# Optimization experiments

Measured on AMD Instinct MI355X. Metric: run time of the kernel, lower is better.

The kernel has to match this reference:

```python
import math
import jax, jax.numpy as jnp
import numpy as np

EMBED_DIM = 1024
NUM_HEADS = 16
FACTOR = 5


def setup_inputs() -> dict:
    key = jax.random.key(0)
    kx, kw, kb, kow, kob = jax.random.split(key, 5)
    B, S, E = 8, 4096, EMBED_DIM
    scale = 1.0 / math.sqrt(E)
    x = jax.random.normal(kx, (B, S, E), dtype=jnp.float32)
    # nn.MultiheadAttention params: packed in_proj (q,k,v) and out_proj
    in_proj_w = jax.random.uniform(kw, (3 * E, E), dtype=jnp.float32, minval=-scale, maxval=scale)
    in_proj_b = jnp.zeros((3 * E,), dtype=jnp.float32)
    out_w = jax.random.uniform(kow, (E, E), dtype=jnp.float32, minval=-scale, maxval=scale)
    out_b = jnp.zeros((E,), dtype=jnp.float32)
    return {"x": x, "in_proj_w": in_proj_w, "in_proj_b": in_proj_b, "out_w": out_w, "out_b": out_b}


def reference(x, in_proj_w, in_proj_b, out_w, out_b):
    B, S, E = x.shape
    H = NUM_HEADS
    hd = E // H
    k = max(1, int(FACTOR * math.log(S + 1)))
    k = min(k, S)

    # top-k queries by L2 norm of each token
    energy = jnp.linalg.norm(x, axis=-1)            # [B, S]
    _, topk_idx = jax.lax.top_k(energy, k)          # [B, k]

    q_tok = jnp.take_along_axis(x, topk_idx[..., None], axis=1)  # [B, k, E]

    Wq, Wk, Wv = jnp.split(in_proj_w, 3, axis=0)    # each [E, E]
    bq, bk, bv = jnp.split(in_proj_b, 3, axis=0)

    q = (q_tok @ Wq.T + bq).reshape(B, k, H, hd)    # [B, k, H, hd]
    kk = (x @ Wk.T + bk).reshape(B, S, H, hd)       # [B, S, H, hd]
    v = (x @ Wv.T + bv).reshape(B, S, H, hd)

    scores = jnp.einsum("bqhd,bshd->bhqs", q, kk) / math.sqrt(hd)
    attn = jax.nn.softmax(scores, axis=-1)          # [B, H, k, S]
    ctx = jnp.einsum("bhqs,bshd->bqhd", attn, v).reshape(B, k, E)
    out_sel = ctx @ out_w.T + out_b                 # [B, k, E]

    # default value for non-selected positions: per-batch mean of x
    default = jnp.mean(x, axis=1)                   # [B, E]
    result = jnp.broadcast_to(default[:, None, :], (B, S, E))
    batch_ar = jnp.arange(B)[:, None]
    result = result.at[batch_ar, topk_idx].set(out_sel)
    return result
```

## Files before the change

### kernel.cpp

```cpp
#include <hip/hip_runtime.h>

using u16 = unsigned short;
using u32 = unsigned int;
using u64 = unsigned long long;
typedef __attribute__((ext_vector_type(8))) short s16x8;
typedef __attribute__((ext_vector_type(4))) short s16x4;
typedef __attribute__((ext_vector_type(4))) float f32x4;

__device__ __forceinline__ float bf2f(u16 u){ return __uint_as_float(((u32)u)<<16); }
__device__ __forceinline__ u16 f2bf(float f){
  u32 u = __float_as_uint(f);
  u += 0x7fffu + ((u>>16)&1u);
  return (u16)(u>>16);
}
__device__ __forceinline__ void gl_lds16(const void* g, void* l){
  __builtin_amdgcn_global_load_lds((const __attribute__((address_space(1))) void*)g,
                                   (__attribute__((address_space(3))) void*)l, 16, 0, 0);
}

__global__ __launch_bounds__(256) void k_cvt_all(const float* __restrict__ ipw, const float* __restrict__ ipb,
                                                 const float* __restrict__ outw, const float* __restrict__ outb,
                                                 u16* __restrict__ ipwb, u16* __restrict__ ipbb,
                                                 u16* __restrict__ outwb, u16* __restrict__ outbb){
  int bid = blockIdx.x;
  const float* src; u16* dst; int n; int base;
  if (bid < 3072){ src=ipw; dst=ipwb; n=3145728; base=bid; }
  else if (bid < 3075){ src=ipb; dst=ipbb; n=3072; base=bid-3072; }
  else if (bid < 4099){ src=outw; dst=outwb; n=1048576; base=bid-3075; }
  else { src=outb; dst=outbb; n=1024; base=0; }
  int i = (base*256 + threadIdx.x)*4;
  if (i >= n) return;
  float4 v = *(const float4*)(src + i);
  s16x4 o;
  o[0]=(short)f2bf(v.x); o[1]=(short)f2bf(v.y); o[2]=(short)f2bf(v.z); o[3]=(short)f2bf(v.w);
  *(s16x4*)(dst + i) = o;
}

__global__ __launch_bounds__(256) void k_prep_x(const float* __restrict__ x, u16* __restrict__ xb, float* __restrict__ energy){
  int tok = blockIdx.x*4 + (threadIdx.x>>6);
  int lane = threadIdx.x & 63;
  const float* p = x + (size_t)tok*1024 + lane*16;
  float4 a[4];
  #pragma unroll
  for (int j=0;j<4;++j) a[j] = ((const float4*)p)[j];
  float s = 0.f;
  s16x8 o0, o1;
  #pragma unroll
  for (int j=0;j<2;++j){
    o0[j*4+0]=(short)f2bf(a[j].x); o0[j*4+1]=(short)f2bf(a[j].y);
    o0[j*4+2]=(short)f2bf(a[j].z); o0[j*4+3]=(short)f2bf(a[j].w);
  }
  #pragma unroll
  for (int j=0;j<2;++j){
    o1[j*4+0]=(short)f2bf(a[2+j].x); o1[j*4+1]=(short)f2bf(a[2+j].y);
    o1[j*4+2]=(short)f2bf(a[2+j].z); o1[j*4+3]=(short)f2bf(a[2+j].w);
  }
  #pragma unroll
  for (int j=0;j<4;++j){
    s += a[j].x*a[j].x + a[j].y*a[j].y + a[j].z*a[j].z + a[j].w*a[j].w;
  }
  u16* xo = xb + (size_t)tok*1024 + lane*16;
  *(s16x8*)xo = o0;
  *(s16x8*)(xo+8) = o1;
  #pragma unroll
  for (int off=32; off; off>>=1) s += __shfl_xor(s, off);
  if (lane==0) energy[tok] = s;
}

__global__ __launch_bounds__(256) void k_colsum(const u16* __restrict__ xb, float* __restrict__ colsum){
  int b = blockIdx.x, sc = blockIdx.y;
  int t = threadIdx.x;
  float acc[4] = {0.f,0.f,0.f,0.f};
  for (int s = sc*128; s < sc*128+128; ++s){
    s16x4 v = *(const s16x4*)(xb + ((size_t)b*4096 + s)*1024 + t*4);
    #pragma unroll
    for (int i=0;i<4;++i) acc[i] += bf2f((u16)v[i]);
  }
  #pragma unroll
  for (int i=0;i<4;++i) atomicAdd(&colsum[b*1024 + t*4 + i], acc[i]);
}

__global__ __launch_bounds__(256) void k_topk(const float* __restrict__ energy, int* __restrict__ topk, int* __restrict__ sel){
  int b = blockIdx.x, t = threadIdx.x;
  int lane = t & 63, wid = t >> 6;
  __shared__ u64 wmax[4];
  __shared__ u64 winner;
  u64 v[16];
  #pragma unroll
  for (int i=0;i<16;++i){
    u32 tok = i*256 + t;
    float e = energy[b*4096 + tok];
    v[i] = ((u64)__float_as_uint(e) << 32) | (u32)(~tok);
    sel[b*4096 + tok] = -1;
  }
  __syncthreads();
  for (int it=0; it<41; ++it){
    u64 m = v[0];
    #pragma unroll
    for (int i=1;i<16;++i) m = v[i] > m ? v[i] : m;
    #pragma unroll
    for (int off=32; off; off>>=1){
      u64 o = __shfl_xor(m, off);
      m = o > m ? o : m;
    }
    if (lane==0) wmax[wid] = m;
    __syncthreads();
    if (t==0){
      u64 g = wmax[0];
      #pragma unroll
      for (int w=1;w<4;++w) g = wmax[w] > g ? wmax[w] : g;
      winner = g;
      u32 tok = (~(u32)g) & 4095u;
      topk[b*64+it] = (int)tok;
      sel[b*4096 + tok] = it;
    }
    __syncthreads();
    u32 wtok = (~(u32)winner) & 4095u;
    #pragma unroll
    for (int i=0;i<16;++i){
      if ((u32)(i*256 + t) == wtok) v[i] = 0;
    }
  }
}

__global__ __launch_bounds__(256) void k_gather_q(const float* __restrict__ x, const int* __restrict__ topk,
                                                  u16* __restrict__ Aq){
  int b = blockIdx.x, qi = blockIdx.y, t = threadIdx.x;
  size_t dst = ((size_t)(b*48+qi))*1024 + t*4;
  if (qi >= 41){ s16x4 z = {0,0,0,0}; *(s16x4*)&Aq[dst] = z; return; }
  int tok = topk[b*64+qi];
  float4 v = *(const float4*)(x + ((size_t)b*4096 + tok)*1024 + t*4);
  s16x4 o;
  o[0]=(short)f2bf(v.x); o[1]=(short)f2bf(v.y); o[2]=(short)f2bf(v.z); o[3]=(short)f2bf(v.w);
  *(s16x4*)&Aq[dst] = o;
}

__global__ __launch_bounds__(256) void k_gemm(const u16* __restrict__ A, const u16* __restrict__ Bk,
                                              const u16* __restrict__ Bv,
                                              const u16* __restrict__ biask, const u16* __restrict__ biasv,
                                              u16* __restrict__ C, int nbn, int ncols, int half, float cscale){
  __shared__ u16 As[128*64];
  __shared__ u16 Bs[128*64];
  const int tid = threadIdx.x;
  const int bn = blockIdx.x % nbn;
  const int bm = blockIdx.x / nbn;
  const int m0 = bm*128, n0 = bn*128;
  const u16* Bbase  = (n0 < half) ? (Bk + (size_t)n0*1024) : (Bv + (size_t)(n0-half)*1024);
  const u16* biasp  = (n0 < half) ? (biask + n0) : (biasv + (n0-half));
  const int lane = tid & 63;
  const int wave = tid >> 6;
  const int wr = wave >> 1, wc = wave & 1;
  const int fr = lane & 15;
  const int fq = lane >> 4;
  f32x4 acc[4][4] = {};
  for (int k0 = 0; k0 < 1024; k0 += 64){
    __syncthreads();
    #pragma unroll
    for (int j=0;j<4;++j){
      int idx = j*256 + tid;
      int r = idx>>3; int cc = (idx&7)*8;
      gl_lds16(A + (size_t)(m0+r)*1024 + k0 + cc, &As[r*64+cc]);
    }
    #pragma unroll
    for (int j=0;j<4;++j){
      int idx = j*256 + tid;
      int r = idx>>3; int cc = (idx&7)*8;
      gl_lds16(Bbase + (size_t)r*1024 + k0 + cc, &Bs[r*64+cc]);
    }
    __syncthreads();
    #pragma unroll
    for (int kk=0; kk<64; kk+=32){
      s16x8 af[4], bfv[4];
      #pragma unroll
      for (int m=0;m<4;++m) af[m] = *(const s16x8*)&As[(wr*64 + m*16 + fr)*64 + kk + fq*8];
      #pragma unroll
      for (int n=0;n<4;++n) bfv[n] = *(const s16x8*)&Bs[(wc*64 + n*16 + fr)*64 + kk + fq*8];
      #pragma unroll
      for (int m=0;m<4;++m)
        #pragma unroll
        for (int n=0;n<4;++n)
          acc[m][n] = __builtin_amdgcn_mfma_f32_16x16x32_bf16(af[m], bfv[n], acc[m][n], 0,0,0);
    }
  }
  #pragma unroll
  for (int n=0;n<4;++n){
    int cl = wc*64 + n*16 + fr;
    int col = n0 + cl;
    float bvv = bf2f(biasp[cl]);
    #pragma unroll
    for (int m=0;m<4;++m){
      int rowb = m0 + wr*64 + m*16 + fq*4;
      f32x4 v = acc[m][n];
      #pragma unroll
      for (int i=0;i<4;++i)
        C[(size_t)(rowb+i)*ncols + col] = f2bf((v[i]+bvv)*cscale);
    }
  }
}

__device__ __forceinline__ void stageA2(const u16* __restrict__ A, int m0, int k0, u16* ldsSlot, int tid){
  #pragma unroll
  for (int j=0;j<4;++j){
    int idx = j*512 + tid;
    int row = idx>>3;
    int chunk = (tid&7) ^ (row&7);
    gl_lds16(A + (size_t)(m0+row)*1024 + k0 + chunk*8, ldsSlot + (size_t)idx*8);
  }
}
__device__ __forceinline__ void stageB2(const u16* __restrict__ B, int k0, u16* ldsSlot, int tid){
  #pragma unroll
  for (int j=0;j<2;++j){
    int idx = j*512 + tid;
    int row = idx>>3;
    int chunk = (tid&7) ^ (row&7);
    gl_lds16(B + (size_t)row*1024 + k0 + chunk*8, ldsSlot + 16384 + (size_t)idx*8);
  }
}
__device__ __forceinline__ s16x8 fragA2(const u16* slot, int row, int k2, int fq){
  int chunk = (fq + k2*4) ^ (row&7);
  return *(const s16x8*)(slot + row*64 + chunk*8);
}
__device__ __forceinline__ s16x8 fragB2(const u16* slot, int row, int k2, int fq){
  int chunk = (fq + k2*4) ^ (row&7);
  return *(const s16x8*)(slot + 16384 + row*64 + chunk*8);
}

__global__ __launch_bounds__(512) void k_kvgemm2(const u16* __restrict__ A, const u16* __restrict__ Bk,
                                                 const u16* __restrict__ Bv,
                                                 const u16* __restrict__ biask, const u16* __restrict__ biasv,
                                                 u16* __restrict__ C){
  __shared__ u16 lds[3*24576];
  const int tid = threadIdx.x;
  const int sbid = (blockIdx.x & 7)*256 + (blockIdx.x >> 3);
  const int bn = sbid & 15;
  const int bm = sbid >> 4;
  const int m0 = bm*256, n0 = bn*128;
  const u16* Bbase = (bn < 8) ? (Bk + (size_t)n0*1024) : (Bv + (size_t)(n0-1024)*1024);
  const u16* biasp = (bn < 8) ? (biask + n0) : (biasv + (n0-1024));
  const int lane = tid & 63, wid = tid >> 6;
  const int wm = wid >> 1, wn = wid & 1;
  const int fr = lane & 15, fq = lane >> 4;
  f32x4 acc[4][4] = {};

  stageA2(A, m0, 0, lds, tid);        stageB2(Bbase, 0, lds, tid);
  stageA2(A, m0, 64, lds+24576, tid); stageB2(Bbase, 64, lds+24576, tid);
  asm volatile("s_waitcnt vmcnt(6)" ::: "memory");
  __builtin_amdgcn_s_barrier();

  for (int t=0; t<16; ++t){
    const u16* slot = lds + (t%3)*24576;
    u16* nslot = (u16*)lds + ((t+2)%3)*24576;
    if (t < 14){ stageA2(A, m0, (t+2)*64, nslot, tid); stageB2(Bbase, (t+2)*64, nslot, tid); }
    s16x8 afr[4][2], bfr[4][2];
    #pragma unroll
    for (int m=0;m<4;++m)
      #pragma unroll
      for (int k2=0;k2<2;++k2)
        afr[m][k2] = fragA2(slot, wm*64 + m*16 + fr, k2, fq);
    #pragma unroll
    for (int n=0;n<4;++n)
      #pragma unroll
      for (int k2=0;k2<2;++k2)
        bfr[n][k2] = fragB2(slot, wn*64 + n*16 + fr, k2, fq);
    __builtin_amdgcn_s_setprio(1);
    #pragma unroll
    for (int m=0;m<4;++m)
      #pragma unroll
      for (int n=0;n<4;++n)
        #pragma unroll
        for (int k2=0;k2<2;++k2)
          acc[m][n] = __builtin_amdgcn_mfma_f32_16x16x32_bf16(afr[m][k2], bfr[n][k2], acc[m][n], 0,0,0);
    __builtin_amdgcn_s_setprio(0);
    if (t < 14){
      asm volatile("s_waitcnt vmcnt(6)" ::: "memory");
    } else if (t == 14){
      asm volatile("s_waitcnt vmcnt(0)" ::: "memory");
    }
    __builtin_amdgcn_s_barrier();
  }

  #pragma unroll
  for (int n=0;n<4;++n){
    int cl = wn*64 + n*16 + fr;
    int col = n0 + cl;
    float bvv = bf2f(biasp[cl]);
    #pragma unroll
    for (int m=0;m<4;++m){
      int rowb = m0 + wm*64 + m*16 + fq*4;
      f32x4 v = acc[m][n];
      #pragma unroll
      for (int i=0;i<4;++i)
        C[(size_t)(rowb+i)*2048 + col] = f2bf(v[i]+bvv);
    }
  }
}

__global__ __launch_bounds__(64) void k_attn(const u16* __restrict__ qb, const u16* __restrict__ KV,
                                             float* __restrict__ part_ctx, float* __restrict__ part_ml,
                                             int G, int hg0, int ncols, int half, int nt, int NSP){
  const int b = blockIdx.x / G, hl = blockIdx.x % G;
  const int h = hg0 + hl;
  const int bh = b*16 + h;
  const int sp = blockIdx.y;
  const int lane = threadIdx.x;
  const int fr = lane & 15, fq = lane >> 4;
  __shared__ u16 k_lds[64*72];
  __shared__ u16 v_lds[64*72];
  __shared__ u16 p_lds[48*72];
  s16x8 af[3][2];
  #pragma unroll
  for (int m=0;m<3;++m)
    #pragma unroll
    for (int kk=0;kk<2;++kk)
      af[m][kk] = *(const s16x8*)(qb + ((size_t)(b*48 + m*16 + fr))*1024 + h*64 + kk*32 + fq*8);
  f32x4 acc_o[3][4] = {};
  float m_run[3][4], l_run[3][4];
  #pragma unroll
  for (int m=0;m<3;++m)
    #pragma unroll
    for (int i=0;i<4;++i){ m_run[m][i] = -3e38f; l_run[m][i] = 0.f; }

  for (int it=0; it<nt; ++it){
    int s0 = (sp*nt + it)*64;
    __syncthreads();
    #pragma unroll
    for (int j=0;j<8;++j){
      int r = j*8 + (lane>>3);
      int sg = (lane&7)*8;
      const u16* kp = KV + ((size_t)(b*4096 + s0 + r))*ncols + hl*64 + sg;
      *(s16x8*)&k_lds[r*72+sg] = *(const s16x8*)kp;
      *(s16x8*)&v_lds[r*72+sg] = *(const s16x8*)(kp+half);
    }
    __syncthreads();
    f32x4 sc4[3][4] = {};
    #pragma unroll
    for (int kk=0;kk<2;++kk){
      s16x8 bk[4];
      #pragma unroll
      for (int n=0;n<4;++n)
        bk[n] = *(const s16x8*)&k_lds[(n*16+fr)*72 + kk*32 + fq*8];
      #pragma unroll
      for (int m=0;m<3;++m)
        #pragma unroll
        for (int n=0;n<4;++n)
          sc4[m][n] = __builtin_amdgcn_mfma_f32_16x16x32_bf16(af[m][kk], bk[n], sc4[m][n], 0,0,0);
    }
    #pragma unroll
    for (int m=0;m<3;++m){
      #pragma unroll
      for (int i=0;i<4;++i){
        float rmax = fmaxf(fmaxf(sc4[m][0][i], sc4[m][1][i]), fmaxf(sc4[m][2][i], sc4[m][3][i]));
        #pragma unroll
        for (int off=1; off<16; off<<=1) rmax = fmaxf(rmax, __shfl_xor(rmax, off));
        float mnew = fmaxf(m_run[m][i], rmax);
        float alpha = __expf(m_run[m][i] - mnew);
        m_run[m][i] = mnew;
        float rsum = 0.f;
        #pragma unroll
        for (int n=0;n<4;++n){
          float p = __expf(sc4[m][n][i] - mnew);
          rsum += p;
          p_lds[(m*16 + fq*4 + i)*72 + n*16 + fr] = f2bf(p);
        }
        #pragma unroll
        for (int off=1; off<16; off<<=1) rsum += __shfl_xor(rsum, off);
        l_run[m][i] = l_run[m][i]*alpha + rsum;
        #pragma unroll
        for (int n=0;n<4;++n) acc_o[m][n][i] *= alpha;
      }
    }
    __syncthreads();
    #pragma unroll
    for (int kk=0;kk<2;++kk){
      s16x8 ap[3];
      #pragma unroll
      for (int m=0;m<3;++m)
        ap[m] = *(const s16x8*)&p_lds[(m*16+fr)*72 + kk*32 + fq*8];
      #pragma unroll
      for (int n=0;n<4;++n){
        s16x8 bv;
        #pragma unroll
        for (int i2=0;i2<8;++i2)
          bv[i2] = (short)v_lds[(kk*32 + fq*8 + i2)*72 + n*16 + fr];
        #pragma unroll
        for (int m=0;m<3;++m)
          acc_o[m][n] = __builtin_amdgcn_mfma_f32_16x16x32_bf16(ap[m], bv, acc_o[m][n], 0,0,0);
      }
    }
  }
  size_t pbase = ((size_t)(bh*NSP + sp))*48*64;
  #pragma unroll
  for (int m=0;m<3;++m)
    #pragma unroll
    for (int n=0;n<4;++n)
      #pragma unroll
      for (int i=0;i<4;++i){
        int qi = m*16 + fq*4 + i, d = n*16 + fr;
        part_ctx[pbase + (size_t)qi*64 + d] = acc_o[m][n][i];
      }
  if (fr==0){
    #pragma unroll
    for (int m=0;m<3;++m)
      #pragma unroll
      for (int i=0;i<4;++i){
        int qi = m*16 + fq*4 + i;
        part_ml[((size_t)(bh*NSP+sp))*96 + qi*2+0] = m_run[m][i];
        part_ml[((size_t)(bh*NSP+sp))*96 + qi*2+1] = l_run[m][i];
      }
  }
}

__global__ __launch_bounds__(64) void k_combine(const float* __restrict__ part_ctx, const float* __restrict__ part_ml,
                                                u16* __restrict__ ctxb, int NSP){
  int bh = blockIdx.x, qi = blockIdx.y;
  int b = bh>>4, h = bh&15;
  int lane = threadIdx.x;
  size_t dst = ((size_t)(b*48+qi))*1024 + h*64 + lane;
  if (qi >= 41){ ctxb[dst] = 0; return; }
  float M = -3e38f;
  for (int p=0;p<NSP;++p)
    M = fmaxf(M, part_ml[((size_t)(bh*NSP+p))*96 + qi*2+0]);
  float l = 0.f, c = 0.f;
  for (int p=0;p<NSP;++p){
    float pm = part_ml[((size_t)(bh*NSP+p))*96 + qi*2+0];
    float pl = part_ml[((size_t)(bh*NSP+p))*96 + qi*2+1];
    float w = __expf(pm-M);
    l += pl*w;
    c += w * part_ctx[((size_t)(bh*NSP+p))*48*64 + (size_t)qi*64 + lane];
  }
  ctxb[dst] = f2bf(c / l);
}

__global__ __launch_bounds__(256) void k_finalize(const u16* __restrict__ outg, const float* __restrict__ colsum,
                                                  const int* __restrict__ sel, float* __restrict__ out){
  int row = blockIdx.x;
  int b = row >> 12;
  int t = threadIdx.x;
  int s = sel[row];
  float4 o;
  if (s >= 0){
    s16x4 v = *(const s16x4*)&outg[((size_t)(b*48+s))*1024 + t*4];
    o.x = bf2f((u16)v[0]); o.y = bf2f((u16)v[1]); o.z = bf2f((u16)v[2]); o.w = bf2f((u16)v[3]);
  } else {
    o = *(const float4*)(colsum + b*1024 + t*4);
    o.x *= (1.f/4096.f); o.y *= (1.f/4096.f); o.z *= (1.f/4096.f); o.w *= (1.f/4096.f);
  }
  *(float4*)(out + (size_t)row*1024 + t*4) = o;
}

extern "C" void kernel_launch(void* const* d_in, const int* in_sizes, int n_in,
                              void* d_out, int out_size, void* d_ws, size_t ws_size,
                              hipStream_t stream) {
  const float* x    = (const float*)d_in[0];
  const float* ipw  = (const float*)d_in[1];
  const float* ipb  = (const float*)d_in[2];
  const float* outw = (const float*)d_in[3];
  const float* outb = (const float*)d_in[4];
  float* out = (float*)d_out;
  char* ws = (char*)d_ws;

  const int cfgG[7]   = {16, 8, 4, 2, 1, 1, 1};
  const int cfgNSP[7] = {16,16,16,16,16, 4, 2};
  int G = 1, NSP = 2;
  size_t oXB=0,oWIP=0,oBIP=0,oWO=0,oBO=0,oEN=0,oCS=0,oTK=0,oSEL=0,oAQ=0,oQB=0,oCTXB=0,oOG=0,oPML=0,oPCTX=0,oKV=0;
  for (int ci=0; ci<7; ++ci){
    int g = cfgG[ci], nsp = cfgNSP[ci];
    size_t o = 0;
    size_t xb=o;   o += 67108864;
    size_t wip=o;  o += 6291456;
    size_t bip=o;  o += 6144;
    size_t wo=o;   o += 2097152;
    size_t bo=o;   o += 2048;
    size_t en=o;   o += 131072;
    size_t cs=o;   o += 32768;
    size_t tk=o;   o += 2048;
    size_t sl=o;   o += 131072;
    size_t aq=o;   o += 786432;
    size_t qb=o;   o += 786432;
    size_t cb=o;   o += 786432;
    size_t og=o;   o += 786432;
    size_t pm=o;   o += (size_t)nsp*49152;
    size_t pc=o;   o += (size_t)nsp*1572864;
    size_t kv=o;   o += (size_t)g*8388608;
    if (o <= ws_size || ci == 6){
      G=g; NSP=nsp;
      oXB=xb; oWIP=wip; oBIP=bip; oWO=wo; oBO=bo; oEN=en; oCS=cs; oTK=tk; oSEL=sl;
      oAQ=aq; oQB=qb; oCTXB=cb; oOG=og; oPML=pm; oPCTX=pc; oKV=kv;
      break;
    }
  }

  u16*   xb     = (u16*)(ws + oXB);
  u16*   ipwb   = (u16*)(ws + oWIP);
  u16*   ipbb   = (u16*)(ws + oBIP);
  u16*   outwb  = (u16*)(ws + oWO);
  u16*   outbb  = (u16*)(ws + oBO);
  float* energy = (float*)(ws + oEN);
  float* colsum = (float*)(ws + oCS);
  int*   topk   = (int*)(ws + oTK);
  int*   sel    = (int*)(ws + oSEL);
  u16*   Aq     = (u16*)(ws + oAQ);
  u16*   qbf    = (u16*)(ws + oQB);
  u16*   ctxb   = (u16*)(ws + oCTXB);
  u16*   outg   = (u16*)(ws + oOG);
  float* pml    = (float*)(ws + oPML);
  float* pctx   = (float*)(ws + oPCTX);
  u16*   KV     = (u16*)(ws + oKV);

  hipMemsetAsync(colsum, 0, 8*1024*sizeof(float), stream);

  k_cvt_all <<<4100, 256, 0, stream>>>(ipw, ipb, outw, outb, ipwb, ipbb, outwb, outbb);

  k_prep_x <<<8192, 256, 0, stream>>>(x, xb, energy);
  k_colsum <<<dim3(8,32), 256, 0, stream>>>(xb, colsum);
  k_topk   <<<8, 256, 0, stream>>>(energy, topk, sel);
  k_gather_q<<<dim3(8,48), 256, 0, stream>>>(x, topk, Aq);

  k_gemm <<<24, 256, 0, stream>>>(Aq, ipwb, ipwb, ipbb, ipbb, qbf, 8, 1024, 1024, 0.125f);

  if (G == 16){
    const int nt = 64/NSP;
    k_kvgemm2 <<<2048, 512, 0, stream>>>(xb,
        ipwb + (size_t)1024*1024, ipwb + (size_t)2048*1024,
        ipbb + 1024, ipbb + 2048, KV);
    k_attn <<<dim3(128, NSP), 64, 0, stream>>>(qbf, KV, pctx, pml, 16, 0, 2048, 1024, nt, NSP);
  } else {
    const int nchunk = 16 / G;
    const int ncols = G*128, half = G*64, nt = 64/NSP;
    for (int c=0; c<nchunk; ++c){
      int hg0 = c*G;
      k_gemm <<<G*256, 256, 0, stream>>>(
          xb,
          ipwb + (size_t)(1024 + hg0*64)*1024,
          ipwb + (size_t)(2048 + hg0*64)*1024,
          ipbb + 1024 + hg0*64,
          ipbb + 2048 + hg0*64,
          KV, G, ncols, half, 1.0f);
      k_attn <<<dim3(8*G, NSP), 64, 0, stream>>>(qbf, KV, pctx, pml, G, hg0, ncols, half, nt, NSP);
    }
  }

  k_combine<<<dim3(128,48), 64, 0, stream>>>(pctx, pml, ctxb, NSP);

  k_gemm <<<24, 256, 0, stream>>>(ctxb, outwb, outwb, outbb, outbb, outg, 8, 1024, 1024, 1.0f);

  k_finalize<<<32768, 256, 0, stream>>>(outg, colsum, sel, out);
}
```

Baseline: 413.9 us.

## Retile KV GEMM to 256x256 with split-phase loads and split-K small GEMMs

The fused K/V projection GEMM now uses 256x256 output tiles with a K-step of 32 and a triple-buffered LDS ring. Global-to-LDS staging for A and B is interleaved between two halves of the MFMA work, with barriers between them, to raise arithmetic intensity per tile. The small Q and output projections switch to a split-K kernel that accumulates into fp32 buffers with atomics, followed by a bias/scale finish pass, to spread these 24-block GEMMs over more CUs. This adds memsets and atomic traffic, and makes the output bias an fp32 add.

```diff
diff --git a/kernel.cpp b/kernel.cpp
--- a/kernel.cpp
+++ b/kernel.cpp
@@ -19,15 +19,14 @@
 }
 
 __global__ __launch_bounds__(256) void k_cvt_all(const float* __restrict__ ipw, const float* __restrict__ ipb,
-                                                 const float* __restrict__ outw, const float* __restrict__ outb,
+                                                 const float* __restrict__ outw,
                                                  u16* __restrict__ ipwb, u16* __restrict__ ipbb,
-                                                 u16* __restrict__ outwb, u16* __restrict__ outbb){
+                                                 u16* __restrict__ outwb){
   int bid = blockIdx.x;
   const float* src; u16* dst; int n; int base;
   if (bid < 3072){ src=ipw; dst=ipwb; n=3145728; base=bid; }
   else if (bid < 3075){ src=ipb; dst=ipbb; n=3072; base=bid-3072; }
-  else if (bid < 4099){ src=outw; dst=outwb; n=1048576; base=bid-3075; }
-  else { src=outb; dst=outbb; n=1024; base=0; }
+  else { src=outw; dst=outwb; n=1048576; base=bid-3075; }
   int i = (base*256 + threadIdx.x)*4;
   if (i >= n) return;
   float4 v = *(const float4*)(src + i);
@@ -198,85 +197,172 @@
   }
 }
 
-__device__ __forceinline__ void stageA2(const u16* __restrict__ A, int m0, int k0, u16* ldsSlot, int tid){
-  #pragma unroll
-  for (int j=0;j<4;++j){
-    int idx = j*512 + tid;
-    int row = idx>>3;
-    int chunk = (tid&7) ^ (row&7);
-    gl_lds16(A + (size_t)(m0+row)*1024 + k0 + chunk*8, ldsSlot + (size_t)idx*8);
-  }
-}
-__device__ __forceinline__ void stageB2(const u16* __restrict__ B, int k0, u16* ldsSlot, int tid){
+__global__ __launch_bounds__(256) void k_gemm_sk(const u16* __restrict__ A, const u16* __restrict__ B,
+                                                 float* __restrict__ Cacc){
+  __shared__ u16 As[128*64];
+  __shared__ u16 Bs[128*64];
+  const int tid = threadIdx.x;
+  const int bn = blockIdx.x & 7;
+  const int bm = blockIdx.x >> 3;
+  const int kc = blockIdx.y;
+  const int m0 = bm*128, n0 = bn*128;
+  const u16* Bbase = B + (size_t)n0*1024;
+  const int lane = tid & 63;
+  const int wave = tid >> 6;
+  const int wr = wave >> 1, wc = wave & 1;
+  const int fr = lane & 15;
+  const int fq = lane >> 4;
+  f32x4 acc[4][4] = {};
+  for (int k0 = kc*256; k0 < kc*256+256; k0 += 64){
+    __syncthreads();
+    #pragma unroll
+    for (int j=0;j<4;++j){
+      int idx = j*256 + tid;
+      int r = idx>>3; int cc = (idx&7)*8;
+      gl_lds16(A + (size_t)(m0+r)*1024 + k0 + cc, &As[r*64+cc]);
+    }
+    #pragma unroll
+    for (int j=0;j<4;++j){
+      int idx = j*256 + tid;
+      int r = idx>>3; int cc = (idx&7)*8;
+      gl_lds16(Bbase + (size_t)r*1024 + k0 + cc, &Bs[r*64+cc]);
+    }
+    __syncthreads();
+    #pragma unroll
+    for (int kk=0; kk<64; kk+=32){
+      s16x8 af[4], bfv[4];
+      #pragma unroll
+      for (int m=0;m<4;++m) af[m] = *(const s16x8*)&As[(wr*64 + m*16 + fr)*64 + kk + fq*8];
+      #pragma unroll
+      for (int n=0;n<4;++n) bfv[n] = *(const s16x8*)&Bs[(wc*64 + n*16 + fr)*64 + kk + fq*8];
+      #pragma unroll
+      for (int m=0;m<4;++m)
+        #pragma unroll
+        for (int n=0;n<4;++n)
+          acc[m][n] = __builtin_amdgcn_mfma_f32_16x16x32_bf16(af[m], bfv[n], acc[m][n], 0,0,0);
+    }
+  }
+  #pragma unroll
+  for (int n=0;n<4;++n){
+    int col = n0 + wc*64 + n*16 + fr;
+    #pragma unroll
+    for (int m=0;m<4;++m){
+      int rowb = m0 + wr*64 + m*16 + fq*4;
+      f32x4 v = acc[m][n];
+      #pragma unroll
+      for (int i=0;i<4;++i)
+        atomicAdd(&Cacc[(size_t)(rowb+i)*1024 + col], v[i]);
+    }
+  }
+}
+
+__global__ __launch_bounds__(256) void k_qfinish(const float* __restrict__ qacc, const float* __restrict__ ipb,
+                                                 u16* __restrict__ qbf){
+  int i = (blockIdx.x*256 + threadIdx.x)*4;
+  float4 a = *(const float4*)(qacc + i);
+  int col = i & 1023;
+  float4 bq = *(const float4*)(ipb + col);
+  s16x4 o;
+  o[0]=(short)f2bf((a.x+bq.x)*0.125f);
+  o[1]=(short)f2bf((a.y+bq.y)*0.125f);
+  o[2]=(short)f2bf((a.z+bq.z)*0.125f);
+  o[3]=(short)f2bf((a.w+bq.w)*0.125f);
+  *(s16x4*)(qbf + i) = o;
+}
+
+__device__ __forceinline__ void stageA3(const u16* __restrict__ A, int m0, int k0, u16* slot, int tid){
   #pragma unroll
   for (int j=0;j<2;++j){
     int idx = j*512 + tid;
-    int row = idx>>3;
-    int chunk = (tid&7) ^ (row&7);
-    gl_lds16(B + (size_t)row*1024 + k0 + chunk*8, ldsSlot + 16384 + (size_t)idx*8);
-  }
-}
-__device__ __forceinline__ s16x8 fragA2(const u16* slot, int row, int k2, int fq){
-  int chunk = (fq + k2*4) ^ (row&7);
-  return *(const s16x8*)(slot + row*64 + chunk*8);
-}
-__device__ __forceinline__ s16x8 fragB2(const u16* slot, int row, int k2, int fq){
-  int chunk = (fq + k2*4) ^ (row&7);
-  return *(const s16x8*)(slot + 16384 + row*64 + chunk*8);
-}
-
-__global__ __launch_bounds__(512) void k_kvgemm2(const u16* __restrict__ A, const u16* __restrict__ Bk,
+    int row = idx>>2;
+    int sc = (idx&3) ^ ((row>>1)&3);
+    gl_lds16(A + (size_t)(m0+row)*1024 + k0 + sc*8, slot + (size_t)idx*8);
+  }
+}
+__device__ __forceinline__ void stageB3(const u16* __restrict__ B, int k0, u16* slot, int tid){
+  #pragma unroll
+  for (int j=0;j<2;++j){
+    int idx = j*512 + tid;
+    int row = idx>>2;
+    int sc = (idx&3) ^ ((row>>1)&3);
+    gl_lds16(B + (size_t)row*1024 + k0 + sc*8, slot + 8192 + (size_t)idx*8);
+  }
+}
+__device__ __forceinline__ s16x8 fragA3(const u16* slot, int row, int fq){
+  int pc = fq ^ ((row>>1)&3);
+  return *(const s16x8*)(slot + row*32 + pc*8);
+}
+__device__ __forceinline__ s16x8 fragB3(const u16* slot, int row, int fq){
+  int pc = fq ^ ((row>>1)&3);
+  return *(const s16x8*)(slot + 8192 + row*32 + pc*8);
+}
+
+__global__ __launch_bounds__(512) void k_kvgemm3(const u16* __restrict__ A, const u16* __restrict__ Bk,
                                                  const u16* __restrict__ Bv,
                                                  const u16* __restrict__ biask, const u16* __restrict__ biasv,
                                                  u16* __restrict__ C){
-  __shared__ u16 lds[3*24576];
+  __shared__ u16 lds[3*16384];
   const int tid = threadIdx.x;
-  const int sbid = (blockIdx.x & 7)*256 + (blockIdx.x >> 3);
-  const int bn = sbid & 15;
-  const int bm = sbid >> 4;
-  const int m0 = bm*256, n0 = bn*128;
-  const u16* Bbase = (bn < 8) ? (Bk + (size_t)n0*1024) : (Bv + (size_t)(n0-1024)*1024);
-  const u16* biasp = (bn < 8) ? (biask + n0) : (biasv + (n0-1024));
+  const int sbid = ((int)blockIdx.x & 7)*128 + ((int)blockIdx.x >> 3);
+  const int bn = sbid & 7;
+  const int bm = sbid >> 3;
+  const int m0 = bm*256, n0 = bn*256;
+  const u16* Bbase = (bn < 4) ? (Bk + (size_t)n0*1024) : (Bv + (size_t)(n0-1024)*1024);
+  const u16* biasp = (bn < 4) ? (biask + n0) : (biasv + (n0-1024));
   const int lane = tid & 63, wid = tid >> 6;
-  const int wm = wid >> 1, wn = wid & 1;
+  const int wm = wid >> 2, wn = wid & 3;
   const int fr = lane & 15, fq = lane >> 4;
-  f32x4 acc[4][4] = {};
-
-  stageA2(A, m0, 0, lds, tid);        stageB2(Bbase, 0, lds, tid);
-  stageA2(A, m0, 64, lds+24576, tid); stageB2(Bbase, 64, lds+24576, tid);
-  asm volatile("s_waitcnt vmcnt(6)" ::: "memory");
+  f32x4 acc[8][4] = {};
+
+  stageA3(A, m0, 0, lds, tid);          stageB3(Bbase, 0, lds, tid);
+  stageA3(A, m0, 32, lds+16384, tid);   stageB3(Bbase, 32, lds+16384, tid);
+  asm volatile("s_waitcnt vmcnt(4)" ::: "memory");
   __builtin_amdgcn_s_barrier();
-
-  for (int t=0; t<16; ++t){
-    const u16* slot = lds + (t%3)*24576;
-    u16* nslot = (u16*)lds + ((t+2)%3)*24576;
-    if (t < 14){ stageA2(A, m0, (t+2)*64, nslot, tid); stageB2(Bbase, (t+2)*64, nslot, tid); }
-    s16x8 afr[4][2], bfr[4][2];
+  __builtin_amdgcn_sched_barrier(0);
+
+  for (int t=0; t<32; ++t){
+    const u16* slot = lds + (t%3)*16384;
+    u16* nslot = (u16*)lds + ((t+2)%3)*16384;
+    s16x8 afr[8], bfr[4];
+    #pragma unroll
+    for (int m=0;m<4;++m) afr[m] = fragA3(slot, wm*128 + m*16 + fr, fq);
+    #pragma unroll
+    for (int n=0;n<4;++n) bfr[n] = fragB3(slot, wn*64 + n*16 + fr, fq);
+    if (t < 30) stageA3(A, m0, (t+2)*32, nslot, tid);
+    __builtin_amdgcn_sched_barrier(0);
+    __builtin_amdgcn_s_barrier();
+    __builtin_amdgcn_sched_barrier(0);
+    __builtin_amdgcn_s_setprio(1);
     #pragma unroll
     for (int m=0;m<4;++m)
       #pragma unroll
-      for (int k2=0;k2<2;++k2)
-        afr[m][k2] = fragA2(slot, wm*64 + m*16 + fr, k2, fq);
-    #pragma unroll
-    for (int n=0;n<4;++n)
-      #pragma unroll
-      for (int k2=0;k2<2;++k2)
-        bfr[n][k2] = fragB2(slot, wn*64 + n*16 + fr, k2, fq);
+      for (int n=0;n<4;++n)
+        acc[m][n] = __builtin_amdgcn_mfma_f32_16x16x32_bf16(afr[m], bfr[n], acc[m][n], 0,0,0);
+    __builtin_amdgcn_s_setprio(0);
+    __builtin_amdgcn_sched_barrier(0);
+    __builtin_amdgcn_s_barrier();
+    __builtin_amdgcn_sched_barrier(0);
+    #pragma unroll
+    for (int m=4;m<8;++m) afr[m] = fragA3(slot, wm*128 + m*16 + fr, fq);
+    if (t < 30) stageB3(Bbase, (t+2)*32, nslot, tid);
+    __builtin_amdgcn_sched_barrier(0);
+    __builtin_amdgcn_s_barrier();
+    __builtin_amdgcn_sched_barrier(0);
     __builtin_amdgcn_s_setprio(1);
     #pragma unroll
-    for (int m=0;m<4;++m)
+    for (int m=4;m<8;++m)
       #pragma unroll
       for (int n=0;n<4;++n)
-        #pragma unroll
-        for (int k2=0;k2<2;++k2)
-          acc[m][n] = __builtin_amdgcn_mfma_f32_16x16x32_bf16(afr[m][k2], bfr[n][k2], acc[m][n], 0,0,0);
+        acc[m][n] = __builtin_amdgcn_mfma_f32_16x16x32_bf16(afr[m], bfr[n], acc[m][n], 0,0,0);
     __builtin_amdgcn_s_setprio(0);
-    if (t < 14){
-      asm volatile("s_waitcnt vmcnt(6)" ::: "memory");
-    } else if (t == 14){
+    if (t < 30){
+      asm volatile("s_waitcnt vmcnt(4)" ::: "memory");
+    } else if (t == 30){
       asm volatile("s_waitcnt vmcnt(0)" ::: "memory");
     }
+    __builtin_amdgcn_sched_barrier(0);
     __builtin_amdgcn_s_barrier();
+    __builtin_amdgcn_sched_barrier(0);
   }
 
   #pragma unroll
@@ -285,8 +371,8 @@
     int col = n0 + cl;
     float bvv = bf2f(biasp[cl]);
     #pragma unroll
-    for (int m=0;m<4;++m){
-      int rowb = m0 + wm*64 + m*16 + fq*4;
+    for (int m=0;m<8;++m){
+      int rowb = m0 + wm*128 + m*16 + fq*4;
       f32x4 v = acc[m][n];
       #pragma unroll
       for (int i=0;i<4;++i)
@@ -431,7 +517,8 @@
   ctxb[dst] = f2bf(c / l);
 }
 
-__global__ __launch_bounds__(256) void k_finalize(const u16* __restrict__ outg, const float* __restrict__ colsum,
+__global__ __launch_bounds__(256) void k_finalize(const float* __restrict__ oacc, const float* __restrict__ outb,
+                                                  const float* __restrict__ colsum,
                                                   const int* __restrict__ sel, float* __restrict__ out){
   int row = blockIdx.x;
   int b = row >> 12;
@@ -439,8 +526,9 @@
   int s = sel[row];
   float4 o;
   if (s >= 0){
-    s16x4 v = *(const s16x4*)&outg[((size_t)(b*48+s))*1024 + t*4];
-    o.x = bf2f((u16)v[0]); o.y = bf2f((u16)v[1]); o.z = bf2f((u16)v[2]); o.w = bf2f((u16)v[3]);
+    float4 a = *(const float4*)(oacc + ((size_t)(b*48+s))*1024 + t*4);
+    float4 bb = *(const float4*)(outb + t*4);
+    o.x = a.x+bb.x; o.y = a.y+bb.y; o.z = a.z+bb.z; o.w = a.w+bb.w;
   } else {
     o = *(const float4*)(colsum + b*1024 + t*4);
     o.x *= (1.f/4096.f); o.y *= (1.f/4096.f); o.z *= (1.f/4096.f); o.w *= (1.f/4096.f);
@@ -462,7 +550,7 @@
   const int cfgG[7]   = {16, 8, 4, 2, 1, 1, 1};
   const int cfgNSP[7] = {16,16,16,16,16, 4, 2};
   int G = 1, NSP = 2;
-  size_t oXB=0,oWIP=0,oBIP=0,oWO=0,oBO=0,oEN=0,oCS=0,oTK=0,oSEL=0,oAQ=0,oQB=0,oCTXB=0,oOG=0,oPML=0,oPCTX=0,oKV=0;
+  size_t oXB=0,oWIP=0,oBIP=0,oWO=0,oEN=0,oCS=0,oTK=0,oSEL=0,oAQ=0,oQB=0,oCTXB=0,oQA=0,oOA=0,oPML=0,oPCTX=0,oKV=0;
   for (int ci=0; ci<7; ++ci){
     int g = cfgG[ci], nsp = cfgNSP[ci];
     size_t o = 0;
@@ -470,7 +558,6 @@
     size_t wip=o;  o += 6291456;
     size_t bip=o;  o += 6144;
     size_t wo=o;   o += 2097152;
-    size_t bo=o;   o += 2048;
     size_t en=o;   o += 131072;
     size_t cs=o;   o += 32768;
     size_t tk=o;   o += 2048;
@@ -478,14 +565,15 @@
     size_t aq=o;   o += 786432;
     size_t qb=o;   o += 786432;
     size_t cb=o;   o += 786432;
-    size_t og=o;   o += 786432;
+    size_t qa=o;   o += 1572864;
+    size_t oa=o;   o += 1572864;
     size_t pm=o;   o += (size_t)nsp*49152;
     size_t pc=o;   o += (size_t)nsp*1572864;
     size_t kv=o;   o += (size_t)g*8388608;
     if (o <= ws_size || ci == 6){
       G=g; NSP=nsp;
-      oXB=xb; oWIP=wip; oBIP=bip; oWO=wo; oBO=bo; oEN=en; oCS=cs; oTK=tk; oSEL=sl;
-      oAQ=aq; oQB=qb; oCTXB=cb; oOG=og; oPML=pm; oPCTX=pc; oKV=kv;
+      oXB=xb; oWIP=wip; oBIP=bip; oWO=wo; oEN=en; oCS=cs; oTK=tk; oSEL=sl;
+      oAQ=aq; oQB=qb; oCTXB=cb; oQA=qa; oOA=oa; oPML=pm; oPCTX=pc; oKV=kv;
       break;
     }
   }
@@ -494,7 +582,6 @@
   u16*   ipwb   = (u16*)(ws + oWIP);
   u16*   ipbb   = (u16*)(ws + oBIP);
   u16*   outwb  = (u16*)(ws + oWO);
-  u16*   outbb  = (u16*)(ws + oBO);
   float* energy = (float*)(ws + oEN);
   float* colsum = (float*)(ws + oCS);
   int*   topk   = (int*)(ws + oTK);
@@ -502,25 +589,29 @@
   u16*   Aq     = (u16*)(ws + oAQ);
   u16*   qbf    = (u16*)(ws + oQB);
   u16*   ctxb   = (u16*)(ws + oCTXB);
-  u16*   outg   = (u16*)(ws + oOG);
+  float* qacc   = (float*)(ws + oQA);
+  float* oacc   = (float*)(ws + oOA);
   float* pml    = (float*)(ws + oPML);
   float* pctx   = (float*)(ws + oPCTX);
   u16*   KV     = (u16*)(ws + oKV);
 
-  hipMemsetAsync(colsum, 0, 8*1024*sizeof(float), stream);
-
-  k_cvt_all <<<4100, 256, 0, stream>>>(ipw, ipb, outw, outb, ipwb, ipbb, outwb, outbb);
+  hipMemsetAsync(colsum, 0, 32768, stream);
+  hipMemsetAsync(qacc, 0, 1572864, stream);
+  hipMemsetAsync(oacc, 0, 1572864, stream);
+
+  k_cvt_all <<<4099, 256, 0, stream>>>(ipw, ipb, outw, ipwb, ipbb, outwb);
 
   k_prep_x <<<8192, 256, 0, stream>>>(x, xb, energy);
   k_colsum <<<dim3(8,32), 256, 0, stream>>>(xb, colsum);
   k_topk   <<<8, 256, 0, stream>>>(energy, topk, sel);
   k_gather_q<<<dim3(8,48), 256, 0, stream>>>(x, topk, Aq);
 
-  k_gemm <<<24, 256, 0, stream>>>(Aq, ipwb, ipwb, ipbb, ipbb, qbf, 8, 1024, 1024, 0.125f);
+  k_gemm_sk <<<dim3(24,4), 256, 0, stream>>>(Aq, ipwb, qacc);
+  k_qfinish <<<384, 256, 0, stream>>>(qacc, ipb, qbf);
 
   if (G == 16){
     const int nt = 64/NSP;
-    k_kvgemm2 <<<2048, 512, 0, stream>>>(xb,
+    k_kvgemm3 <<<1024, 512, 0, stream>>>(xb,
         ipwb + (size_t)1024*1024, ipwb + (size_t)2048*1024,
         ipbb + 1024, ipbb + 2048, KV);
     k_attn <<<dim3(128, NSP), 64, 0, stream>>>(qbf, KV, pctx, pml, 16, 0, 2048, 1024, nt, NSP);
@@ -542,7 +633,7 @@
 
   k_combine<<<dim3(128,48), 64, 0, stream>>>(pctx, pml, ctxb, NSP);
 
-  k_gemm <<<24, 256, 0, stream>>>(ctxb, outwb, outwb, outbb, outbb, outg, 8, 1024, 1024, 1.0f);
-
-  k_finalize<<<32768, 256, 0, stream>>>(outg, colsum, sel, out);
-}
+  k_gemm_sk <<<dim3(24,4), 256, 0, stream>>>(ctxb, outwb, oacc);
+
+  k_finalize<<<32768, 256, 0, stream>>>(oacc, outb, colsum, sel, out);
+}
```

Result: no change. 410.5 us (-0.8%).
